# Kernel optimization log

Hardware: AMD Instinct MI355X
Metric: run time of the kernel (lower is better)

Reference implementation:

```python
import jax, jax.numpy as jnp
import numpy as np

# torch.optim.Adam defaults
LR = 1e-3
B1 = 0.9
B2 = 0.999
EPS = 1e-8


def setup_inputs() -> dict:
    key = jax.random.key(0)
    k1, k2 = jax.random.split(key)
    B, N_train, d = 128, 16384, 1024
    h = jax.random.normal(k1, (B, d), dtype=jnp.float32)
    H_train = jax.random.normal(k2, (N_train, d), dtype=jnp.float32)
    return {"h": h, "H_train": H_train, "n_epoch": 1000}


def reference(h, H_train, n_epoch):
    # preweights: [B, N_train], optimized by Adam for n_epoch steps
    B, N_train = h.shape[0], H_train.shape[0]

    def loss_fn(p):
        w = jax.nn.softmax(p, axis=-1)          # [B, N_train]
        H_approx = w @ H_train                   # [B, d]
        return jnp.sum((H_approx - h) ** 2)

    grad_fn = jax.grad(loss_fn)

    def step(carry, t):
        p, m, v = carry
        g = grad_fn(p)
        m = B1 * m + (1.0 - B1) * g
        v = B2 * v + (1.0 - B2) * (g * g)
        m_hat = m / (1.0 - B1 ** t)
        v_hat = v / (1.0 - B2 ** t)
        p = p - LR * m_hat / (jnp.sqrt(v_hat) + EPS)
        return (p, m, v), None

    z = jnp.zeros((B, N_train), dtype=jnp.float32)
    ts = jnp.arange(1, n_epoch + 1, dtype=jnp.float32)
    (p, _, _), _ = jax.lax.scan(step, (z, z, z), ts)
    return jax.nn.softmax(p, axis=-1)
```

## Files before the change

### kernel.cpp

```cpp
#include <hip/hip_runtime.h>
#include <math.h>

#define BB 128
#define NTR 16384
#define DD 1024
#define PN (BB*NTR)
#define CN (BB*DD)
#define HN (NTR*DD)
#define FWD_SLABS 64
#define BWD_SLABS 2

typedef short bf16x8 __attribute__((ext_vector_type(8)));
typedef float f32x2  __attribute__((ext_vector_type(2)));
typedef float f32x4v __attribute__((ext_vector_type(4)));

__device__ __forceinline__ ushort f2bf(float f) {
  uint u = __float_as_uint(f);
  return (ushort)((u + 0x7FFFu + ((u >> 16) & 1u)) >> 16);
}
__device__ __forceinline__ float bf2f(ushort h) { return __uint_as_float(((uint)h) << 16); }
__device__ __forceinline__ void split2(float f, ushort& a, ushort& b) {
  a = f2bf(f); float r1 = f - bf2f(a);
  b = f2bf(r1);
}

__global__ __launch_bounds__(256) void k_prep(const float* __restrict__ H,
    ushort* __restrict__ H0, ushort* __restrict__ H1)
{
  const size_t i = ((size_t)blockIdx.x * 256 + threadIdx.x) * 4;
  const float4 x = *(const float4*)(H + i);
  ushort a[4], b[4];
  split2(x.x, a[0], b[0]); split2(x.y, a[1], b[1]);
  split2(x.z, a[2], b[2]); split2(x.w, a[3], b[3]);
  *(ushort4*)(H0 + i) = make_ushort4(a[0], a[1], a[2], a[3]);
  *(ushort4*)(H1 + i) = make_ushort4(b[0], b[1], b[2], b[3]);
}

__global__ __launch_bounds__(256) void k_softmax_f(const float* __restrict__ p,
                                                   float* __restrict__ w) {
  const int row = blockIdx.x, tid = threadIdx.x;
  const float* pr = p + (size_t)row * NTR;
  float x[64]; float mx = -INFINITY;
#pragma unroll
  for (int i = 0; i < 64; ++i) { x[i] = pr[i*256 + tid]; mx = fmaxf(mx, x[i]); }
  __shared__ float red[256];
  red[tid] = mx; __syncthreads();
  for (int s = 128; s > 0; s >>= 1) { if (tid < s) red[tid] = fmaxf(red[tid], red[tid+s]); __syncthreads(); }
  mx = red[0]; __syncthreads();
  float sum = 0.f;
#pragma unroll
  for (int i = 0; i < 64; ++i) { x[i] = expf(x[i] - mx); sum += x[i]; }
  red[tid] = sum; __syncthreads();
  for (int s = 128; s > 0; s >>= 1) { if (tid < s) red[tid] += red[tid+s]; __syncthreads(); }
  const float inv = 1.0f / red[0];
  float* wr = w + (size_t)row * NTR;
#pragma unroll
  for (int i = 0; i < 64; ++i) wr[i*256 + tid] = x[i] * inv;
}

__global__ __launch_bounds__(256) void k_fwd_v(const float* __restrict__ w,
    const float* __restrict__ H, float* __restrict__ Cp)
{
  const int nt = blockIdx.x, tid = threadIdx.x;
  const int kbase = blockIdx.y * 256;
  Cp += (size_t)blockIdx.y * CN;
  __shared__ float As[8][128];
  __shared__ float Bs[8][128];
  const int tm = tid >> 4, tn = tid & 15;
  const int m0 = tm * 8, n0 = tn * 8;
  f32x2 acc[8][4];
#pragma unroll
  for (int i = 0; i < 8; ++i)
#pragma unroll
    for (int j = 0; j < 4; ++j) acc[i][j] = (f32x2){0.f, 0.f};
  for (int kk = 0; kk < 256; kk += 8) {
    {
      const int mm = tid >> 1, q = tid & 1;
      const float4 a4 = *(const float4*)(w + (size_t)mm*NTR + kbase + kk + q*4);
      As[q*4+0][mm]=a4.x; As[q*4+1][mm]=a4.y; As[q*4+2][mm]=a4.z; As[q*4+3][mm]=a4.w;
    }
    {
      const int r = tid >> 5, c = (tid & 31) * 4;
      *(float4*)&Bs[r][c] = *(const float4*)(H + (size_t)(kbase+kk+r)*DD + nt*128 + c);
    }
    __syncthreads();
#pragma unroll
    for (int k = 0; k < 8; ++k) {
      float a[8];
      *(float4*)&a[0] = *(const float4*)&As[k][m0];
      *(float4*)&a[4] = *(const float4*)&As[k][m0+4];
      f32x2 b[4];
      b[0] = *(const f32x2*)&Bs[k][n0];
      b[1] = *(const f32x2*)&Bs[k][n0+2];
      b[2] = *(const f32x2*)&Bs[k][n0+4];
      b[3] = *(const f32x2*)&Bs[k][n0+6];
#pragma unroll
      for (int i = 0; i < 8; ++i) {
        const f32x2 ai = (f32x2){a[i], a[i]};
#pragma unroll
        for (int j = 0; j < 4; ++j)
          acc[i][j] = __builtin_elementwise_fma(ai, b[j], acc[i][j]);
      }
    }
    __syncthreads();
  }
#pragma unroll
  for (int i = 0; i < 8; ++i) {
    float* dst = Cp + (size_t)(m0+i)*DD + nt*128 + n0;
    *(float4*)dst     = make_float4(acc[i][0].x, acc[i][0].y, acc[i][1].x, acc[i][1].y);
    *(float4*)(dst+4) = make_float4(acc[i][2].x, acc[i][2].y, acc[i][3].x, acc[i][3].y);
  }
}

__global__ __launch_bounds__(256) void k_reduce_S2s(const float* __restrict__ X,
    const float* __restrict__ h,
    ushort* __restrict__ s0, ushort* __restrict__ s1)
{
  const size_t off = ((size_t)blockIdx.x * 256 + threadIdx.x) * 4;
  float4 s = make_float4(0.f, 0.f, 0.f, 0.f);
#pragma unroll 4
  for (int k = 0; k < FWD_SLABS; ++k) {
    const float4 c = *(const float4*)(X + (size_t)k * CN + off);
    s.x += c.x; s.y += c.y; s.z += c.z; s.w += c.w;
  }
  const float4 hh = *(const float4*)(h + off);
  float vals[4] = {2.f*(s.x-hh.x), 2.f*(s.y-hh.y), 2.f*(s.z-hh.z), 2.f*(s.w-hh.w)};
  ushort a[4], b[4];
#pragma unroll
  for (int e = 0; e < 4; ++e) split2(vals[e], a[e], b[e]);
  *(ushort4*)(s0 + off) = make_ushort4(a[0], a[1], a[2], a[3]);
  *(ushort4*)(s1 + off) = make_ushort4(b[0], b[1], b[2], b[3]);
}

__global__ __launch_bounds__(256, 2) void k_gemm3_bwd(
    const ushort* __restrict__ A0, const ushort* __restrict__ A1,
    const ushort* __restrict__ B0, const ushort* __restrict__ B1,
    const float* __restrict__ w,
    float* __restrict__ C, float* __restrict__ rpart)
{
  __shared__ ushort lds[16384];
  __shared__ float rbuf[128][33];
  const int tid = threadIdx.x;
  const int lane = tid & 63, wid = tid >> 6;
  const int wm = (wid >> 1) * 64, wn = (wid & 1) * 64;
  const int bn = blockIdx.x, ks = blockIdx.y;
  const int n0 = bn * 128;
  const int kbase = ks * 512;
  C += (size_t)ks * PN;

  const ushort* Ap[2] = {A0, A1};
  const ushort* Bp[2] = {B0, B1};

  f32x4v acc[4][4];
#pragma unroll
  for (int i = 0; i < 4; ++i)
#pragma unroll
    for (int j = 0; j < 4; ++j) acc[i][j] = (f32x4v){0.f, 0.f, 0.f, 0.f};

  for (int kt = 0; kt < 16; ++kt) {
    const int kpos = kbase + (kt << 5);
#pragma unroll
    for (int c = 0; c < 4; ++c) {
      const int L = c*256 + tid;
      const int s = L >> 9, rr = L & 511;
      const int row = rr >> 2, slot = rr & 3;
      const int sl = slot ^ ((row >> 1) & 3);
      const ushort* src = Ap[s] + (size_t)row * DD + kpos + (sl << 3);
      __builtin_amdgcn_global_load_lds((const __attribute__((address_space(1))) void*)src,
          (__attribute__((address_space(3))) void*)&lds[(size_t)(c*256 + (wid << 6)) * 8], 16, 0, 0);
    }
#pragma unroll
    for (int c = 0; c < 4; ++c) {
      const int L = c*256 + tid;
      const int s = L >> 9, rr = L & 511;
      const int row = rr >> 2, slot = rr & 3;
      const int sl = slot ^ ((row >> 1) & 3);
      const ushort* src = Bp[s] + (size_t)(n0 + row) * DD + kpos + (sl << 3);
      __builtin_amdgcn_global_load_lds((const __attribute__((address_space(1))) void*)src,
          (__attribute__((address_space(3))) void*)&lds[8192 + (size_t)(c*256 + (wid << 6)) * 8], 16, 0, 0);
    }
    __syncthreads();

    bf16x8 bf[2][4];
#pragma unroll
    for (int s = 0; s < 2; ++s)
#pragma unroll
      for (int j = 0; j < 4; ++j) {
        const int n = wn + j*16 + (lane & 15);
        const int sl = (lane >> 4) ^ ((n >> 1) & 3);
        bf[s][j] = *(const bf16x8*)&lds[8192 + s*4096 + n*32 + sl*8];
      }
#pragma unroll
    for (int sa = 0; sa < 2; ++sa) {
      bf16x8 af[4];
#pragma unroll
      for (int i = 0; i < 4; ++i) {
        const int mrow = wm + i*16 + (lane & 15);
        const int sl = (lane >> 4) ^ ((mrow >> 1) & 3);
        af[i] = *(const bf16x8*)&lds[sa*4096 + mrow*32 + sl*8];
      }
#pragma unroll
      for (int sb = 0; sb < 2 - sa; ++sb)
#pragma unroll
        for (int i = 0; i < 4; ++i)
#pragma unroll
          for (int j = 0; j < 4; ++j)
            acc[i][j] = __builtin_amdgcn_mfma_f32_16x16x32_bf16(af[i], bf[sb][j], acc[i][j], 0, 0, 0);
    }
    __syncthreads();
  }
#pragma unroll
  for (int i = 0; i < 4; ++i) {
    const int rbase = wm + i*16 + ((lane >> 4) << 2);
#pragma unroll
    for (int r = 0; r < 4; ++r) {
      const int row = rbase + r;
      float s = 0.f;
#pragma unroll
      for (int j = 0; j < 4; ++j) {
        const int cg = n0 + wn + j*16 + (lane & 15);
        C[(size_t)row * NTR + cg] = acc[i][j][r];
        s = fmaf(w[(size_t)row * NTR + cg], acc[i][j][r], s);
      }
      rbuf[row][((wid & 1) << 4) + (lane & 15)] = s;
    }
  }
  __syncthreads();
  if (tid < 128) {
    float s = 0.f;
#pragma unroll
    for (int t = 0; t < 32; ++t) s += rbuf[tid][t];
    rpart[((size_t)ks*128 + bn)*128 + tid] = s;
  }
}

__global__ __launch_bounds__(256) void k_adam_f(float* __restrict__ p,
    float* __restrict__ m, float* __restrict__ v,
    const float* __restrict__ w, const float* __restrict__ X,
    const float* __restrict__ rpart, float bc1, float bc2)
{
  const int bid = blockIdx.x, tid = threadIdx.x;
  const int row = bid >> 3;
  __shared__ float red[256];
  red[tid] = rpart[(size_t)tid*128 + row];
  __syncthreads();
  for (int s = 128; s > 0; s >>= 1) { if (tid < s) red[tid] += red[tid+s]; __syncthreads(); }
  const float rr = red[0];
  const size_t base = (size_t)bid * 2048 + tid * 4;
#pragma unroll
  for (int part = 0; part < 2; ++part) {
    const size_t off = base + part * 1024;
    float4 u  = *(const float4*)(X + off);
    const float4 u1 = *(const float4*)(X + (size_t)PN + off);
    u.x += u1.x; u.y += u1.y; u.z += u1.z; u.w += u1.w;
    const float4 w4 = *(const float4*)(w + off);
    const float wv[4] = {w4.x, w4.y, w4.z, w4.w};
    const float uu[4] = {u.x, u.y, u.z, u.w};
    float4 p4 = *(float4*)(p + off);
    float4 m4 = *(float4*)(m + off);
    float4 v4 = *(float4*)(v + off);
    float* pp = (float*)&p4; float* mm = (float*)&m4; float* vv = (float*)&v4;
#pragma unroll
    for (int e = 0; e < 4; ++e) {
      const float g  = wv[e] * (uu[e] - rr);
      const float mn = 0.9f*mm[e] + 0.1f*g;
      const float vn = 0.999f*vv[e] + 0.001f*(g*g);
      const float mh = mn / bc1, vh = vn / bc2;
      pp[e] = pp[e] - 1e-3f * mh / (sqrtf(vh) + 1e-8f);
      mm[e] = mn; vv[e] = vn;
    }
    *(float4*)(p + off) = p4;
    *(float4*)(m + off) = m4;
    *(float4*)(v + off) = v4;
  }
}

extern "C" void kernel_launch(void* const* d_in, const int* in_sizes, int n_in,
                              void* d_out, int out_size, void* d_ws, size_t ws_size,
                              hipStream_t stream) {
  const float* h = (const float*)d_in[0];
  const float* H = (const float*)d_in[1];
  (void)in_sizes; (void)n_in; (void)out_size; (void)ws_size;
  const int n_epoch = 1000;

  float* p  = (float*)d_ws;
  float* m  = p + PN;
  float* v  = m + PN;
  float* w  = v + PN;
  float* X  = w + PN;
  float* rp = X + (size_t)4*PN;
  ushort* s0 = (ushort*)(rp + 256*128);
  ushort* s1 = s0 + CN;
  ushort* H0 = s1 + CN, *H1 = H0 + HN;

  hipMemsetAsync(p, 0, (size_t)3*PN*sizeof(float), stream);
  k_prep<<<HN/1024, 256, 0, stream>>>(H, H0, H1);

  for (int s = 1; s <= n_epoch; ++s) {
    k_softmax_f<<<BB, 256, 0, stream>>>(p, w);
    k_fwd_v<<<dim3(8, FWD_SLABS), 256, 0, stream>>>(w, H, X);
    k_reduce_S2s<<<CN/1024, 256, 0, stream>>>(X, h, s0, s1);
    k_gemm3_bwd<<<dim3(128, BWD_SLABS), 256, 0, stream>>>(s0, s1, H0, H1, w, X, rp);
    const float bc1 = 1.0f - powf(0.9f,   (float)s);
    const float bc2 = 1.0f - powf(0.999f, (float)s);
    k_adam_f<<<1024, 256, 0, stream>>>(p, m, v, w, X, rp, bc1, bc2);
  }
  k_softmax_f<<<BB, 256, 0, stream>>>(p, (float*)d_out);
}
```

Measured before the change: 117.0 ms.

## Increase parallelism across softmax, reduce, backward GEMM and prefetch forward tiles

The softmax now uses 512 threads per row and the slab reduction kernel handles two elements per thread, which launches more blocks. The backward GEMM tile width is halved to 64 columns, giving 512 blocks instead of 256 on the GPU, and the Adam kernel reads twice as many partial row sums to match. The forward fp32 GEMM now prefetches the next tile into registers while computing on the current one. The aim is better occupancy and latency hiding, at the cost of more global loads of the A operand and more partial results in the backward GEMM.

```diff
diff --git a/kernel.cpp b/kernel.cpp
--- a/kernel.cpp
+++ b/kernel.cpp
@@ -36,26 +36,26 @@
   *(ushort4*)(H1 + i) = make_ushort4(b[0], b[1], b[2], b[3]);
 }
 
-__global__ __launch_bounds__(256) void k_softmax_f(const float* __restrict__ p,
+__global__ __launch_bounds__(512) void k_softmax_f(const float* __restrict__ p,
                                                    float* __restrict__ w) {
   const int row = blockIdx.x, tid = threadIdx.x;
   const float* pr = p + (size_t)row * NTR;
-  float x[64]; float mx = -INFINITY;
-#pragma unroll
-  for (int i = 0; i < 64; ++i) { x[i] = pr[i*256 + tid]; mx = fmaxf(mx, x[i]); }
-  __shared__ float red[256];
+  float x[32]; float mx = -INFINITY;
+#pragma unroll
+  for (int i = 0; i < 32; ++i) { x[i] = pr[i*512 + tid]; mx = fmaxf(mx, x[i]); }
+  __shared__ float red[512];
   red[tid] = mx; __syncthreads();
-  for (int s = 128; s > 0; s >>= 1) { if (tid < s) red[tid] = fmaxf(red[tid], red[tid+s]); __syncthreads(); }
+  for (int s = 256; s > 0; s >>= 1) { if (tid < s) red[tid] = fmaxf(red[tid], red[tid+s]); __syncthreads(); }
   mx = red[0]; __syncthreads();
   float sum = 0.f;
 #pragma unroll
-  for (int i = 0; i < 64; ++i) { x[i] = expf(x[i] - mx); sum += x[i]; }
+  for (int i = 0; i < 32; ++i) { x[i] = expf(x[i] - mx); sum += x[i]; }
   red[tid] = sum; __syncthreads();
-  for (int s = 128; s > 0; s >>= 1) { if (tid < s) red[tid] += red[tid+s]; __syncthreads(); }
+  for (int s = 256; s > 0; s >>= 1) { if (tid < s) red[tid] += red[tid+s]; __syncthreads(); }
   const float inv = 1.0f / red[0];
   float* wr = w + (size_t)row * NTR;
 #pragma unroll
-  for (int i = 0; i < 64; ++i) wr[i*256 + tid] = x[i] * inv;
+  for (int i = 0; i < 32; ++i) wr[i*512 + tid] = x[i] * inv;
 }
 
 __global__ __launch_bounds__(256) void k_fwd_v(const float* __restrict__ w,
@@ -68,22 +68,28 @@
   __shared__ float Bs[8][128];
   const int tm = tid >> 4, tn = tid & 15;
   const int m0 = tm * 8, n0 = tn * 8;
+  const int mm = tid >> 1, q = tid & 1;
+  const int br = tid >> 5, bc = (tid & 31) * 4;
+  const float* Asrc = w + (size_t)mm*NTR + kbase + q*4;
+  const float* Bsrc = H + (size_t)(kbase+br)*DD + nt*128 + bc;
+
   f32x2 acc[8][4];
 #pragma unroll
   for (int i = 0; i < 8; ++i)
 #pragma unroll
     for (int j = 0; j < 4; ++j) acc[i][j] = (f32x2){0.f, 0.f};
+
+  float4 ra = *(const float4*)(Asrc);
+  float4 rb = *(const float4*)(Bsrc);
   for (int kk = 0; kk < 256; kk += 8) {
-    {
-      const int mm = tid >> 1, q = tid & 1;
-      const float4 a4 = *(const float4*)(w + (size_t)mm*NTR + kbase + kk + q*4);
-      As[q*4+0][mm]=a4.x; As[q*4+1][mm]=a4.y; As[q*4+2][mm]=a4.z; As[q*4+3][mm]=a4.w;
-    }
-    {
-      const int r = tid >> 5, c = (tid & 31) * 4;
-      *(float4*)&Bs[r][c] = *(const float4*)(H + (size_t)(kbase+kk+r)*DD + nt*128 + c);
-    }
     __syncthreads();
+    As[q*4+0][mm]=ra.x; As[q*4+1][mm]=ra.y; As[q*4+2][mm]=ra.z; As[q*4+3][mm]=ra.w;
+    *(float4*)&Bs[br][bc] = rb;
+    __syncthreads();
+    if (kk + 8 < 256) {
+      ra = *(const float4*)(Asrc + kk + 8);
+      rb = *(const float4*)(Bsrc + (size_t)(kk+8)*DD);
+    }
 #pragma unroll
     for (int k = 0; k < 8; ++k) {
       float a[8];
@@ -102,7 +108,6 @@
           acc[i][j] = __builtin_elementwise_fma(ai, b[j], acc[i][j]);
       }
     }
-    __syncthreads();
   }
 #pragma unroll
   for (int i = 0; i < 8; ++i) {
@@ -116,20 +121,19 @@
     const float* __restrict__ h,
     ushort* __restrict__ s0, ushort* __restrict__ s1)
 {
-  const size_t off = ((size_t)blockIdx.x * 256 + threadIdx.x) * 4;
-  float4 s = make_float4(0.f, 0.f, 0.f, 0.f);
+  const size_t off = ((size_t)blockIdx.x * 256 + threadIdx.x) * 2;
+  f32x2 s = (f32x2){0.f, 0.f};
 #pragma unroll 4
   for (int k = 0; k < FWD_SLABS; ++k) {
-    const float4 c = *(const float4*)(X + (size_t)k * CN + off);
-    s.x += c.x; s.y += c.y; s.z += c.z; s.w += c.w;
-  }
-  const float4 hh = *(const float4*)(h + off);
-  float vals[4] = {2.f*(s.x-hh.x), 2.f*(s.y-hh.y), 2.f*(s.z-hh.z), 2.f*(s.w-hh.w)};
-  ushort a[4], b[4];
-#pragma unroll
-  for (int e = 0; e < 4; ++e) split2(vals[e], a[e], b[e]);
-  *(ushort4*)(s0 + off) = make_ushort4(a[0], a[1], a[2], a[3]);
-  *(ushort4*)(s1 + off) = make_ushort4(b[0], b[1], b[2], b[3]);
+    const f32x2 c = *(const f32x2*)(X + (size_t)k * CN + off);
+    s.x += c.x; s.y += c.y;
+  }
+  const f32x2 hh = *(const f32x2*)(h + off);
+  float v0 = 2.f*(s.x-hh.x), v1 = 2.f*(s.y-hh.y);
+  ushort a0, b0, a1, b1;
+  split2(v0, a0, b0); split2(v1, a1, b1);
+  *(ushort2*)(s0 + off) = make_ushort2(a0, a1);
+  *(ushort2*)(s1 + off) = make_ushort2(b0, b1);
 }
 
 __global__ __launch_bounds__(256, 2) void k_gemm3_bwd(
@@ -138,24 +142,24 @@
     const float* __restrict__ w,
     float* __restrict__ C, float* __restrict__ rpart)
 {
-  __shared__ ushort lds[16384];
+  __shared__ ushort lds[12288];
   __shared__ float rbuf[128][33];
   const int tid = threadIdx.x;
   const int lane = tid & 63, wid = tid >> 6;
-  const int wm = (wid >> 1) * 64, wn = (wid & 1) * 64;
+  const int wm = (wid >> 1) * 64, wn = (wid & 1) * 32;
   const int bn = blockIdx.x, ks = blockIdx.y;
-  const int n0 = bn * 128;
+  const int n0 = bn * 64;
   const int kbase = ks * 512;
   C += (size_t)ks * PN;
 
   const ushort* Ap[2] = {A0, A1};
   const ushort* Bp[2] = {B0, B1};
 
-  f32x4v acc[4][4];
+  f32x4v acc[4][2];
 #pragma unroll
   for (int i = 0; i < 4; ++i)
 #pragma unroll
-    for (int j = 0; j < 4; ++j) acc[i][j] = (f32x4v){0.f, 0.f, 0.f, 0.f};
+    for (int j = 0; j < 2; ++j) acc[i][j] = (f32x4v){0.f, 0.f, 0.f, 0.f};
 
   for (int kt = 0; kt < 16; ++kt) {
     const int kpos = kbase + (kt << 5);
@@ -170,9 +174,9 @@
           (__attribute__((address_space(3))) void*)&lds[(size_t)(c*256 + (wid << 6)) * 8], 16, 0, 0);
     }
 #pragma unroll
-    for (int c = 0; c < 4; ++c) {
+    for (int c = 0; c < 2; ++c) {
       const int L = c*256 + tid;
-      const int s = L >> 9, rr = L & 511;
+      const int s = L >> 8, rr = L & 255;
       const int row = rr >> 2, slot = rr & 3;
       const int sl = slot ^ ((row >> 1) & 3);
       const ushort* src = Bp[s] + (size_t)(n0 + row) * DD + kpos + (sl << 3);
@@ -181,14 +185,14 @@
     }
     __syncthreads();
 
-    bf16x8 bf[2][4];
+    bf16x8 bf[2][2];
 #pragma unroll
     for (int s = 0; s < 2; ++s)
 #pragma unroll
-      for (int j = 0; j < 4; ++j) {
+      for (int j = 0; j < 2; ++j) {
         const int n = wn + j*16 + (lane & 15);
         const int sl = (lane >> 4) ^ ((n >> 1) & 3);
-        bf[s][j] = *(const bf16x8*)&lds[8192 + s*4096 + n*32 + sl*8];
+        bf[s][j] = *(const bf16x8*)&lds[8192 + s*2048 + n*32 + sl*8];
       }
 #pragma unroll
     for (int sa = 0; sa < 2; ++sa) {
@@ -204,7 +208,7 @@
 #pragma unroll
         for (int i = 0; i < 4; ++i)
 #pragma unroll
-          for (int j = 0; j < 4; ++j)
+          for (int j = 0; j < 2; ++j)
             acc[i][j] = __builtin_amdgcn_mfma_f32_16x16x32_bf16(af[i], bf[sb][j], acc[i][j], 0, 0, 0);
     }
     __syncthreads();
@@ -217,12 +221,12 @@
       const int row = rbase + r;
       float s = 0.f;
 #pragma unroll
-      for (int j = 0; j < 4; ++j) {
+      for (int j = 0; j < 2; ++j) {
         const int cg = n0 + wn + j*16 + (lane & 15);
         C[(size_t)row * NTR + cg] = acc[i][j][r];
         s = fmaf(w[(size_t)row * NTR + cg], acc[i][j][r], s);
       }
-      rbuf[row][((wid & 1) << 4) + (lane & 15)] = s;
+      rbuf[row][((wn >> 5) << 4) + (lane & 15)] = s;
     }
   }
   __syncthreads();
@@ -230,7 +234,7 @@
     float s = 0.f;
 #pragma unroll
     for (int t = 0; t < 32; ++t) s += rbuf[tid][t];
-    rpart[((size_t)ks*128 + bn)*128 + tid] = s;
+    rpart[((size_t)ks*256 + bn)*128 + tid] = s;
   }
 }
 
@@ -242,7 +246,7 @@
   const int bid = blockIdx.x, tid = threadIdx.x;
   const int row = bid >> 3;
   __shared__ float red[256];
-  red[tid] = rpart[(size_t)tid*128 + row];
+  red[tid] = rpart[(size_t)tid*128 + row] + rpart[(size_t)(tid+256)*128 + row];
   __syncthreads();
   for (int s = 128; s > 0; s >>= 1) { if (tid < s) red[tid] += red[tid+s]; __syncthreads(); }
   const float rr = red[0];
@@ -289,7 +293,7 @@
   float* w  = v + PN;
   float* X  = w + PN;
   float* rp = X + (size_t)4*PN;
-  ushort* s0 = (ushort*)(rp + 256*128);
+  ushort* s0 = (ushort*)(rp + 512*128);
   ushort* s1 = s0 + CN;
   ushort* H0 = s1 + CN, *H1 = H0 + HN;
 
@@ -297,13 +301,13 @@
   k_prep<<<HN/1024, 256, 0, stream>>>(H, H0, H1);
 
   for (int s = 1; s <= n_epoch; ++s) {
-    k_softmax_f<<<BB, 256, 0, stream>>>(p, w);
+    k_softmax_f<<<BB, 512, 0, stream>>>(p, w);
     k_fwd_v<<<dim3(8, FWD_SLABS), 256, 0, stream>>>(w, H, X);
-    k_reduce_S2s<<<CN/1024, 256, 0, stream>>>(X, h, s0, s1);
-    k_gemm3_bwd<<<dim3(128, BWD_SLABS), 256, 0, stream>>>(s0, s1, H0, H1, w, X, rp);
+    k_reduce_S2s<<<CN/512, 256, 0, stream>>>(X, h, s0, s1);
+    k_gemm3_bwd<<<dim3(256, BWD_SLABS), 256, 0, stream>>>(s0, s1, H0, H1, w, X, rp);
     const float bc1 = 1.0f - powf(0.9f,   (float)s);
     const float bc2 = 1.0f - powf(0.999f, (float)s);
     k_adam_f<<<1024, 256, 0, stream>>>(p, m, v, w, X, rp, bc1, bc2);
   }
-  k_softmax_f<<<BB, 256, 0, stream>>>(p, (float*)d_out);
-}
+  k_softmax_f<<<BB, 512, 0, stream>>>(p, (float*)d_out);
+}
```

After: 110.0 ms. -6.0%, faster.
